# Performance work log

Measured on AMD Instinct MI355X. Metric: run time of the kernel, lower is better.

Reference implementation:

```python
import jax, jax.numpy as jnp
import numpy as np
from jax import lax

LSTM_UNITS = 64
BATCH = 2048
TIMESTEPS = 1024


def _lstm_cell(x, h, c, W_ih, W_hh, b_ih, b_hh):
    # PyTorch LSTMCell gate order: i, f, g, o
    gates = x @ W_ih.T + b_ih + h @ W_hh.T + b_hh
    i, f, g, o = jnp.split(gates, 4, axis=-1)
    c_new = jax.nn.sigmoid(f) * c + jax.nn.sigmoid(i) * jnp.tanh(g)
    h_new = jax.nn.sigmoid(o) * jnp.tanh(c_new)
    return h_new, c_new


def setup_inputs() -> dict:
    key = jax.random.key(0)
    ks = jax.random.split(key, 9)
    U = LSTM_UNITS
    s0 = 1.0 / np.sqrt(U)  # torch LSTMCell init scale (hidden=64)
    s1 = 1.0  # hidden=1 -> scale 1/sqrt(1)
    inp = {
        "input": jax.random.normal(ks[0], (BATCH, TIMESTEPS), dtype=jnp.float32),
        # c0: LSTMCell(1, 64)
        "W_ih0": jax.random.uniform(ks[1], (4 * U, 1), jnp.float32, -s0, s0),
        "W_hh0": jax.random.uniform(ks[2], (4 * U, U), jnp.float32, -s0, s0),
        "b_ih0": jax.random.uniform(ks[3], (4 * U,), jnp.float32, -s0, s0),
        "b_hh0": jax.random.uniform(ks[4], (4 * U,), jnp.float32, -s0, s0),
        # c1: LSTMCell(64, 1)
        "W_ih1": jax.random.uniform(ks[5], (4, U), jnp.float32, -s1, s1),
        "W_hh1": jax.random.uniform(ks[6], (4, 1), jnp.float32, -s1, s1),
        "b_ih1": jax.random.uniform(ks[7], (4,), jnp.float32, -s1, s1),
        "b_hh1": jax.random.uniform(ks[8], (4,), jnp.float32, -s1, s1),
    }
    return inp


def reference(input, W_ih0, W_hh0, b_ih0, b_hh0, W_ih1, W_hh1, b_ih1, b_hh1):
    B = input.shape[0]
    U = LSTM_UNITS
    dt = input.dtype
    h0 = jnp.zeros((B, U), dt)
    c0 = jnp.zeros((B, U), dt)
    h1 = jnp.zeros((B, 1), dt)
    c1 = jnp.zeros((B, 1), dt)

    def step(carry, x_t):
        h0, c0, h1, c1 = carry
        h0n, c0n = _lstm_cell(x_t, h0, c0, W_ih0, W_hh0, b_ih0, b_hh0)
        # NOTE: the original feeds the CELL state c0n (not h0n) into layer 2
        h1n, c1n = _lstm_cell(c0n, h1, c1, W_ih1, W_hh1, b_ih1, b_hh1)
        # output per step is the cell state of layer 2
        return (h0n, c0n, h1n, c1n), c1n

    xs = input.T[:, :, None]  # (T, B, 1)
    _, ys = lax.scan(step, (h0, c0, h1, c1), xs)  # ys: (T, B, 1)
    return ys[:, :, 0].T  # (B, T)
```

## Files before the change

kernel.cpp:

```cpp
#include <hip/hip_runtime.h>

#define T_STEPS 1024
#define BATCH 2048
#define BTILE 4
#define HS 36

typedef short short8 __attribute__((ext_vector_type(8)));
typedef float f32x4 __attribute__((ext_vector_type(4)));
typedef float f32x2 __attribute__((ext_vector_type(2)));

__device__ __forceinline__ float fast_rcp(float x) {
#if __has_builtin(__builtin_amdgcn_rcpf)
    return __builtin_amdgcn_rcpf(x);
#else
    return 1.0f / x;
#endif
}

__device__ __forceinline__ float fast_exp2(float x) {
#if __has_builtin(__builtin_amdgcn_exp2f)
    return __builtin_amdgcn_exp2f(x);
#else
    return exp2f(x);
#endif
}

__device__ __forceinline__ float sigf(float x) {
    return fast_rcp(1.0f + fast_exp2(-1.44269504f * x));
}

__device__ __forceinline__ f32x2 sigf2(f32x2 v) {
    f32x2 t = v * (-1.44269504f);
    f32x2 e = {fast_exp2(t[0]), fast_exp2(t[1])};
    e = e + 1.0f;
    return f32x2{fast_rcp(e[0]), fast_rcp(e[1])};
}

__device__ __forceinline__ float tanh_fast(float x) {
    float e = fast_exp2(2.88539008f * x);
    return 1.0f - 2.0f * fast_rcp(e + 1.0f);
}

__device__ __forceinline__ unsigned f2bf(float x) {
    unsigned u = __float_as_uint(x);
    unsigned r = u + 0x7FFFu + ((u >> 16) & 1u);
    return r >> 16;
}
__device__ __forceinline__ float bf2f(unsigned b) {
    return __uint_as_float(b << 16);
}

__device__ __forceinline__ unsigned cvt_pk_bf16(float a, float b) {
    unsigned r;
    asm("v_cvt_pk_bf16_f32 %0, %1, %2" : "=v"(r) : "v"(a), "v"(b));
    return r;
}

__device__ __forceinline__ float sel4A(f32x4 a) {
    int v = __float_as_int(a[0]);
    v = __builtin_amdgcn_update_dpp(v, __float_as_int(a[1]), 0x114, 0xf, 0x2, false);
    v = __builtin_amdgcn_update_dpp(v, __float_as_int(a[2]), 0x118, 0xf, 0x4, false);
    v = __builtin_amdgcn_update_dpp(v, __float_as_int(a[3]), 0x11C, 0xf, 0x8, false);
    return __int_as_float(v);
}
__device__ __forceinline__ float dpp_shl4f(float v) {
    return __int_as_float(__builtin_amdgcn_update_dpp(0, __float_as_int(v), 0x104, 0xf, 0xf, true));
}

__device__ __forceinline__ void step_barrier() {
    asm volatile("s_waitcnt lgkmcnt(0)" ::: "memory");
    __builtin_amdgcn_s_barrier();
    asm volatile("" ::: "memory");
}

__global__ __launch_bounds__(256, 2)
void lstm_v9_kernel(const float* __restrict__ input,
                    const float* __restrict__ W_ih0,
                    const float* __restrict__ W_hh0,
                    const float* __restrict__ b_ih0,
                    const float* __restrict__ b_hh0,
                    const float* __restrict__ W_ih1,
                    const float* __restrict__ W_hh1,
                    const float* __restrict__ b_ih1,
                    const float* __restrict__ b_hh1,
                    float* __restrict__ out)
{
    const int tid = threadIdx.x;
    const int w   = tid >> 6;
    const int l   = tid & 63;
    const int q16 = l >> 4;
    const int n16 = l & 15;
    const int nb  = l & 3;
    const int r   = (l >> 2) & 3;
    const int u   = 16 * w + 4 * q16 + r;
    const int bbase = blockIdx.x * BTILE;

    __shared__ __align__(16) unsigned Hbuf[2][3][16][HS];
    __shared__ float Xb[2][BTILE][65];
    __shared__ float Lst[8];

    for (int i = tid; i < 2 * 3 * 16 * HS; i += 256)
        reinterpret_cast<unsigned*>(Hbuf)[i] = 0u;
    if (tid < 8) Lst[tid] = 0.0f;

    short8 a1[4][2];
    #pragma unroll
    for (int g = 0; g < 4; ++g) {
        #pragma unroll
        for (int kt = 0; kt < 2; ++kt) {
            const float* p = W_hh0 + (size_t)(16 * (w + 4 * g) + n16) * 64 + kt * 32 + q16 * 8;
            short8 a;
            #pragma unroll
            for (int j = 0; j < 8; ++j) a[j] = (short)f2bf(p[j]);
            a1[g][kt] = a;
        }
    }
    short8 a2h[2], a2l[2];
    #pragma unroll
    for (int kt = 0; kt < 2; ++kt) {
        short8 ah = {0,0,0,0,0,0,0,0}, al = {0,0,0,0,0,0,0,0};
        if (n16 < 4) {
            const float* p = W_ih1 + (size_t)n16 * 64 + kt * 32 + q16 * 8;
            #pragma unroll
            for (int j = 0; j < 8; ++j) {
                unsigned hb = f2bf(p[j]);
                ah[j] = (short)hb;
                al[j] = (short)f2bf(p[j] - bf2f(hb));
            }
        }
        a2h[kt] = ah; a2l[kt] = al;
    }

    f32x2 w01, w23, b01, b23;
    {
        float wgv[4], bgv[4];
        #pragma unroll
        for (int g = 0; g < 4; ++g) {
            int row = g * 64 + u;
            wgv[g] = W_ih0[row];
            bgv[g] = b_ih0[row] + b_hh0[row];
        }
        w01 = f32x2{wgv[0], wgv[1]}; w23 = f32x2{wgv[2], wgv[3]};
        b01 = f32x2{bgv[0], bgv[1]}; b23 = f32x2{bgv[2], bgv[3]};
    }
    float whh1v[4], b1v[4];
    #pragma unroll
    for (int g = 0; g < 4; ++g) { whh1v[g] = W_hh1[g]; b1v[g] = b_ih1[g] + b_hh1[g]; }

    const float* inrow = input + (size_t)(bbase + w) * T_STEPS;
    Xb[0][w][l] = inrow[l];
    float xnext = 0.0f;
    float c0 = 0.0f;

    __syncthreads();

    if (blockIdx.x & 256) {
        __builtin_amdgcn_s_sleep(5);
    }

    int par = 0;
    #pragma unroll 2
    for (int t = 0; t < T_STEPS; ++t) {
        if ((t & 63) == 0 && t + 64 < T_STEPS) xnext = inrow[t + 64 + l];
        const int cp = (t >> 6) & 1;

        const unsigned* Hrow = &Hbuf[par][0][n16][0];
        short8 hb0 = *reinterpret_cast<const short8*>(Hrow + 4 * q16);
        short8 hb1 = *reinterpret_cast<const short8*>(Hrow + 16 + 4 * q16);

        f32x4 accv[4];
        #pragma unroll
        for (int g = 0; g < 4; ++g) {
            f32x4 z = {0.0f, 0.0f, 0.0f, 0.0f};
            z = __builtin_amdgcn_mfma_f32_16x16x32_bf16(a1[g][0], hb0, z, 0, 0, 0);
            z = __builtin_amdgcn_mfma_f32_16x16x32_bf16(a1[g][1], hb1, z, 0, 0, 0);
            accv[g] = z;
        }

        if (t > 0 && w == ((t - 1) & 3)) {
            const unsigned* Ch = &Hbuf[par][1][n16][0];
            const unsigned* Cl = &Hbuf[par][2][n16][0];
            short8 ch0 = *reinterpret_cast<const short8*>(Ch + 4 * q16);
            short8 ch1 = *reinterpret_cast<const short8*>(Ch + 16 + 4 * q16);
            short8 cl0 = *reinterpret_cast<const short8*>(Cl + 4 * q16);
            short8 cl1 = *reinterpret_cast<const short8*>(Cl + 16 + 4 * q16);
            float h1p = Lst[nb], c1p = Lst[4 + nb];
            f32x4 zA = {0.0f, 0.0f, 0.0f, 0.0f};
            f32x4 zB = {0.0f, 0.0f, 0.0f, 0.0f};
            zA = __builtin_amdgcn_mfma_f32_16x16x32_bf16(a2h[0], ch0, zA, 0, 0, 0);
            zB = __builtin_amdgcn_mfma_f32_16x16x32_bf16(a2l[1], ch1, zB, 0, 0, 0);
            zA = __builtin_amdgcn_mfma_f32_16x16x32_bf16(a2h[1], ch1, zA, 0, 0, 0);
            zB = __builtin_amdgcn_mfma_f32_16x16x32_bf16(a2h[0], cl0, zB, 0, 0, 0);
            zA = __builtin_amdgcn_mfma_f32_16x16x32_bf16(a2l[0], ch0, zA, 0, 0, 0);
            zB = __builtin_amdgcn_mfma_f32_16x16x32_bf16(a2h[1], cl1, zB, 0, 0, 0);
            f32x4 z = zA + zB;
            float g1i = z[0] + b1v[0] + h1p * whh1v[0];
            float g1f = z[1] + b1v[1] + h1p * whh1v[1];
            float g1g = z[2] + b1v[2] + h1p * whh1v[2];
            float g1o = z[3] + b1v[3] + h1p * whh1v[3];
            float c1n = sigf(g1f) * c1p + sigf(g1i) * tanh_fast(g1g);
            float h1n = sigf(g1o) * tanh_fast(c1n);
            if (l < 4) {
                out[(size_t)(bbase + l) * T_STEPS + (t - 1)] = c1n;
                Lst[l] = h1n;
                Lst[4 + l] = c1n;
            }
        }

        float g4[4];
        #pragma unroll
        for (int g = 0; g < 4; ++g) g4[g] = sel4A(accv[g]);

        float x = Xb[cp][nb][t & 63];
        f32x2 xx = {x, x};
        f32x2 gif = f32x2{g4[0], g4[1]} + (xx * w01 + b01);
        f32x2 ggo = f32x2{g4[2], g4[3]} + (xx * w23 + b23);

        f32x2 sif = sigf2(gif);
        float tg  = tanh_fast(ggo[0]);
        float c0n = sif[1] * c0 + sif[0] * tg;
        c0 = c0n;
        float h0n = sigf(ggo[1]) * tanh_fast(c0n);

        float ph = dpp_shl4f(h0n);
        float pc = dpp_shl4f(c0n);
        unsigned hword  = cvt_pk_bf16(h0n, ph);
        unsigned chword = cvt_pk_bf16(c0n, pc);
        float hi_own = bf2f(chword & 0xFFFFu);
        float lo_own = c0n - hi_own;
        float plo = dpp_shl4f(lo_own);
        unsigned clword = cvt_pk_bf16(lo_own, plo);
        if (!(l & 4)) {
            int widx = 8 * w + 2 * q16 + (r >> 1);
            Hbuf[par ^ 1][0][nb][widx] = hword;
            Hbuf[par ^ 1][1][nb][widx] = chword;
            Hbuf[par ^ 1][2][nb][widx] = clword;
        }
        if ((t & 63) == 63 && t + 1 < T_STEPS) Xb[cp ^ 1][w][l] = xnext;

        step_barrier();
        par ^= 1;
    }

    if (w == 3) {
        const unsigned* Ch = &Hbuf[par][1][n16][0];
        const unsigned* Cl = &Hbuf[par][2][n16][0];
        short8 ch0 = *reinterpret_cast<const short8*>(Ch + 4 * q16);
        short8 ch1 = *reinterpret_cast<const short8*>(Ch + 16 + 4 * q16);
        short8 cl0 = *reinterpret_cast<const short8*>(Cl + 4 * q16);
        short8 cl1 = *reinterpret_cast<const short8*>(Cl + 16 + 4 * q16);
        float h1p = Lst[nb], c1p = Lst[4 + nb];
        f32x4 zA = {0.0f, 0.0f, 0.0f, 0.0f};
        f32x4 zB = {0.0f, 0.0f, 0.0f, 0.0f};
        zA = __builtin_amdgcn_mfma_f32_16x16x32_bf16(a2h[0], ch0, zA, 0, 0, 0);
        zB = __builtin_amdgcn_mfma_f32_16x16x32_bf16(a2l[1], ch1, zB, 0, 0, 0);
        zA = __builtin_amdgcn_mfma_f32_16x16x32_bf16(a2h[1], ch1, zA, 0, 0, 0);
        zB = __builtin_amdgcn_mfma_f32_16x16x32_bf16(a2h[0], cl0, zB, 0, 0, 0);
        zA = __builtin_amdgcn_mfma_f32_16x16x32_bf16(a2l[0], ch0, zA, 0, 0, 0);
        zB = __builtin_amdgcn_mfma_f32_16x16x32_bf16(a2h[1], cl1, zB, 0, 0, 0);
        f32x4 z = zA + zB;
        float g1i = z[0] + b1v[0] + h1p * whh1v[0];
        float g1f = z[1] + b1v[1] + h1p * whh1v[1];
        float g1g = z[2] + b1v[2] + h1p * whh1v[2];
        float g1o = z[3] + b1v[3] + h1p * whh1v[3];
        float c1n = sigf(g1f) * c1p + sigf(g1i) * tanh_fast(g1g);
        if (l < 4)
            out[(size_t)(bbase + l) * T_STEPS + (T_STEPS - 1)] = c1n;
    }
}

extern "C" void kernel_launch(void* const* d_in, const int* in_sizes, int n_in,
                              void* d_out, int out_size, void* d_ws, size_t ws_size,
                              hipStream_t stream) {
    const float* input = (const float*)d_in[0];
    const float* W_ih0 = (const float*)d_in[1];
    const float* W_hh0 = (const float*)d_in[2];
    const float* b_ih0 = (const float*)d_in[3];
    const float* b_hh0 = (const float*)d_in[4];
    const float* W_ih1 = (const float*)d_in[5];
    const float* W_hh1 = (const float*)d_in[6];
    const float* b_ih1 = (const float*)d_in[7];
    const float* b_hh1 = (const float*)d_in[8];
    float* out = (float*)d_out;

    dim3 grid(BATCH / BTILE);
    dim3 block(256);
    lstm_v9_kernel<<<grid, block, 0, stream>>>(
        input, W_ih0, W_hh0, b_ih0, b_hh0, W_ih1, W_hh1, b_ih1, b_hh1, out);
}
```

Before: 536.7 us.

## Process two interleaved 4-row batch groups per block to hide recurrence latency

Each block now handles 8 batch rows as two independent 4-row streams (A and B) with separate LDS buffers. Their MFMAs and gate math are interleaved so each stream's dependency chain can hide the other's latency. The grid is halved to 256 blocks, launch bounds drop to one block per CU, and the staggered start sleep is removed. Layer-2 work for stream B runs on a different wave than stream A to spread it out. This trades the old two-blocks-per-CU occupancy for instruction-level parallelism inside one block, with higher register pressure.

```diff
diff --git a/kernel.cpp b/kernel.cpp
--- a/kernel.cpp
+++ b/kernel.cpp
@@ -2,7 +2,7 @@
 
 #define T_STEPS 1024
 #define BATCH 2048
-#define BTILE 4
+#define BTILE 8
 #define HS 36
 
 typedef short short8 __attribute__((ext_vector_type(8)));
@@ -73,17 +73,53 @@
     asm volatile("" ::: "memory");
 }
 
-__global__ __launch_bounds__(256, 2)
-void lstm_v9_kernel(const float* __restrict__ input,
-                    const float* __restrict__ W_ih0,
-                    const float* __restrict__ W_hh0,
-                    const float* __restrict__ b_ih0,
-                    const float* __restrict__ b_hh0,
-                    const float* __restrict__ W_ih1,
-                    const float* __restrict__ W_hh1,
-                    const float* __restrict__ b_ih1,
-                    const float* __restrict__ b_hh1,
-                    float* __restrict__ out)
+__device__ __forceinline__ void layer2(const unsigned (*Hb)[16][HS],
+                                       float* Lst,
+                                       const short8* a2h, const short8* a2l,
+                                       const float* whh1v, const float* b1v,
+                                       int n16, int q16, int nb, int l,
+                                       float* out, int bb, int tout)
+{
+    const unsigned* Ch = &Hb[1][n16][0];
+    const unsigned* Cl = &Hb[2][n16][0];
+    short8 ch0 = *reinterpret_cast<const short8*>(Ch + 4 * q16);
+    short8 ch1 = *reinterpret_cast<const short8*>(Ch + 16 + 4 * q16);
+    short8 cl0 = *reinterpret_cast<const short8*>(Cl + 4 * q16);
+    short8 cl1 = *reinterpret_cast<const short8*>(Cl + 16 + 4 * q16);
+    float h1p = Lst[nb], c1p = Lst[4 + nb];
+    f32x4 zA = {0.0f, 0.0f, 0.0f, 0.0f};
+    f32x4 zB = {0.0f, 0.0f, 0.0f, 0.0f};
+    zA = __builtin_amdgcn_mfma_f32_16x16x32_bf16(a2h[0], ch0, zA, 0, 0, 0);
+    zB = __builtin_amdgcn_mfma_f32_16x16x32_bf16(a2l[1], ch1, zB, 0, 0, 0);
+    zA = __builtin_amdgcn_mfma_f32_16x16x32_bf16(a2h[1], ch1, zA, 0, 0, 0);
+    zB = __builtin_amdgcn_mfma_f32_16x16x32_bf16(a2h[0], cl0, zB, 0, 0, 0);
+    zA = __builtin_amdgcn_mfma_f32_16x16x32_bf16(a2l[0], ch0, zA, 0, 0, 0);
+    zB = __builtin_amdgcn_mfma_f32_16x16x32_bf16(a2h[1], cl1, zB, 0, 0, 0);
+    f32x4 z = zA + zB;
+    float g1i = z[0] + b1v[0] + h1p * whh1v[0];
+    float g1f = z[1] + b1v[1] + h1p * whh1v[1];
+    float g1g = z[2] + b1v[2] + h1p * whh1v[2];
+    float g1o = z[3] + b1v[3] + h1p * whh1v[3];
+    float c1n = sigf(g1f) * c1p + sigf(g1i) * tanh_fast(g1g);
+    float h1n = sigf(g1o) * tanh_fast(c1n);
+    if (l < 4) {
+        out[(size_t)(bb + l) * T_STEPS + tout] = c1n;
+        Lst[l] = h1n;
+        Lst[4 + l] = c1n;
+    }
+}
+
+__global__ __launch_bounds__(256, 1)
+void lstm_v10_kernel(const float* __restrict__ input,
+                     const float* __restrict__ W_ih0,
+                     const float* __restrict__ W_hh0,
+                     const float* __restrict__ b_ih0,
+                     const float* __restrict__ b_hh0,
+                     const float* __restrict__ W_ih1,
+                     const float* __restrict__ W_hh1,
+                     const float* __restrict__ b_ih1,
+                     const float* __restrict__ b_hh1,
+                     float* __restrict__ out)
 {
     const int tid = threadIdx.x;
     const int w   = tid >> 6;
@@ -95,13 +131,17 @@
     const int u   = 16 * w + 4 * q16 + r;
     const int bbase = blockIdx.x * BTILE;
 
-    __shared__ __align__(16) unsigned Hbuf[2][3][16][HS];
-    __shared__ float Xb[2][BTILE][65];
-    __shared__ float Lst[8];
-
-    for (int i = tid; i < 2 * 3 * 16 * HS; i += 256)
-        reinterpret_cast<unsigned*>(Hbuf)[i] = 0u;
-    if (tid < 8) Lst[tid] = 0.0f;
+    __shared__ __align__(16) unsigned HbufA[2][3][16][HS];
+    __shared__ __align__(16) unsigned HbufB[2][3][16][HS];
+    __shared__ float XbA[2][4][65];
+    __shared__ float XbB[2][4][65];
+    __shared__ float LstA[8], LstB[8];
+
+    for (int i = tid; i < 2 * 3 * 16 * HS; i += 256) {
+        reinterpret_cast<unsigned*>(HbufA)[i] = 0u;
+        reinterpret_cast<unsigned*>(HbufB)[i] = 0u;
+    }
+    if (tid < 8) { LstA[tid] = 0.0f; LstB[tid] = 0.0f; }
 
     short8 a1[4][2];
     #pragma unroll
@@ -147,126 +187,117 @@
     #pragma unroll
     for (int g = 0; g < 4; ++g) { whh1v[g] = W_hh1[g]; b1v[g] = b_ih1[g] + b_hh1[g]; }
 
-    const float* inrow = input + (size_t)(bbase + w) * T_STEPS;
-    Xb[0][w][l] = inrow[l];
-    float xnext = 0.0f;
-    float c0 = 0.0f;
+    const float* inrowA = input + (size_t)(bbase + w) * T_STEPS;
+    const float* inrowB = input + (size_t)(bbase + 4 + w) * T_STEPS;
+    XbA[0][w][l] = inrowA[l];
+    XbB[0][w][l] = inrowB[l];
+    float xnextA = 0.0f, xnextB = 0.0f;
+    float c0A = 0.0f, c0B = 0.0f;
 
     __syncthreads();
-
-    if (blockIdx.x & 256) {
-        __builtin_amdgcn_s_sleep(5);
-    }
 
     int par = 0;
     #pragma unroll 2
     for (int t = 0; t < T_STEPS; ++t) {
-        if ((t & 63) == 0 && t + 64 < T_STEPS) xnext = inrow[t + 64 + l];
+        if ((t & 63) == 0 && t + 64 < T_STEPS) {
+            xnextA = inrowA[t + 64 + l];
+            xnextB = inrowB[t + 64 + l];
+        }
         const int cp = (t >> 6) & 1;
 
-        const unsigned* Hrow = &Hbuf[par][0][n16][0];
-        short8 hb0 = *reinterpret_cast<const short8*>(Hrow + 4 * q16);
-        short8 hb1 = *reinterpret_cast<const short8*>(Hrow + 16 + 4 * q16);
-
-        f32x4 accv[4];
+        const unsigned* HrA = &HbufA[par][0][n16][0];
+        const unsigned* HrB = &HbufB[par][0][n16][0];
+        short8 hb0A = *reinterpret_cast<const short8*>(HrA + 4 * q16);
+        short8 hb1A = *reinterpret_cast<const short8*>(HrA + 16 + 4 * q16);
+        short8 hb0B = *reinterpret_cast<const short8*>(HrB + 4 * q16);
+        short8 hb1B = *reinterpret_cast<const short8*>(HrB + 16 + 4 * q16);
+
+        f32x4 accA[4], accB[4];
         #pragma unroll
         for (int g = 0; g < 4; ++g) {
-            f32x4 z = {0.0f, 0.0f, 0.0f, 0.0f};
-            z = __builtin_amdgcn_mfma_f32_16x16x32_bf16(a1[g][0], hb0, z, 0, 0, 0);
-            z = __builtin_amdgcn_mfma_f32_16x16x32_bf16(a1[g][1], hb1, z, 0, 0, 0);
-            accv[g] = z;
-        }
-
-        if (t > 0 && w == ((t - 1) & 3)) {
-            const unsigned* Ch = &Hbuf[par][1][n16][0];
-            const unsigned* Cl = &Hbuf[par][2][n16][0];
-            short8 ch0 = *reinterpret_cast<const short8*>(Ch + 4 * q16);
-            short8 ch1 = *reinterpret_cast<const short8*>(Ch + 16 + 4 * q16);
-            short8 cl0 = *reinterpret_cast<const short8*>(Cl + 4 * q16);
-            short8 cl1 = *reinterpret_cast<const short8*>(Cl + 16 + 4 * q16);
-            float h1p = Lst[nb], c1p = Lst[4 + nb];
             f32x4 zA = {0.0f, 0.0f, 0.0f, 0.0f};
             f32x4 zB = {0.0f, 0.0f, 0.0f, 0.0f};
-            zA = __builtin_amdgcn_mfma_f32_16x16x32_bf16(a2h[0], ch0, zA, 0, 0, 0);
-            zB = __builtin_amdgcn_mfma_f32_16x16x32_bf16(a2l[1], ch1, zB, 0, 0, 0);
-            zA = __builtin_amdgcn_mfma_f32_16x16x32_bf16(a2h[1], ch1, zA, 0, 0, 0);
-            zB = __builtin_amdgcn_mfma_f32_16x16x32_bf16(a2h[0], cl0, zB, 0, 0, 0);
-            zA = __builtin_amdgcn_mfma_f32_16x16x32_bf16(a2l[0], ch0, zA, 0, 0, 0);
-            zB = __builtin_amdgcn_mfma_f32_16x16x32_bf16(a2h[1], cl1, zB, 0, 0, 0);
-            f32x4 z = zA + zB;
-            float g1i = z[0] + b1v[0] + h1p * whh1v[0];
-            float g1f = z[1] + b1v[1] + h1p * whh1v[1];
-            float g1g = z[2] + b1v[2] + h1p * whh1v[2];
-            float g1o = z[3] + b1v[3] + h1p * whh1v[3];
-            float c1n = sigf(g1f) * c1p + sigf(g1i) * tanh_fast(g1g);
-            float h1n = sigf(g1o) * tanh_fast(c1n);
-            if (l < 4) {
-                out[(size_t)(bbase + l) * T_STEPS + (t - 1)] = c1n;
-                Lst[l] = h1n;
-                Lst[4 + l] = c1n;
-            }
-        }
-
-        float g4[4];
+            zA = __builtin_amdgcn_mfma_f32_16x16x32_bf16(a1[g][0], hb0A, zA, 0, 0, 0);
+            zB = __builtin_amdgcn_mfma_f32_16x16x32_bf16(a1[g][0], hb0B, zB, 0, 0, 0);
+            zA = __builtin_amdgcn_mfma_f32_16x16x32_bf16(a1[g][1], hb1A, zA, 0, 0, 0);
+            zB = __builtin_amdgcn_mfma_f32_16x16x32_bf16(a1[g][1], hb1B, zB, 0, 0, 0);
+            accA[g] = zA; accB[g] = zB;
+        }
+
+        if (t > 0) {
+            const int lw = (t - 1) & 3;
+            if (w == lw)
+                layer2(HbufA[par], LstA, a2h, a2l, whh1v, b1v,
+                       n16, q16, nb, l, out, bbase, t - 1);
+            if (w == (lw ^ 2))
+                layer2(HbufB[par], LstB, a2h, a2l, whh1v, b1v,
+                       n16, q16, nb, l, out, bbase + 4, t - 1);
+        }
+
+        float g4A[4], g4B[4];
         #pragma unroll
-        for (int g = 0; g < 4; ++g) g4[g] = sel4A(accv[g]);
-
-        float x = Xb[cp][nb][t & 63];
-        f32x2 xx = {x, x};
-        f32x2 gif = f32x2{g4[0], g4[1]} + (xx * w01 + b01);
-        f32x2 ggo = f32x2{g4[2], g4[3]} + (xx * w23 + b23);
-
-        f32x2 sif = sigf2(gif);
-        float tg  = tanh_fast(ggo[0]);
-        float c0n = sif[1] * c0 + sif[0] * tg;
-        c0 = c0n;
-        float h0n = sigf(ggo[1]) * tanh_fast(c0n);
-
-        float ph = dpp_shl4f(h0n);
-        float pc = dpp_shl4f(c0n);
-        unsigned hword  = cvt_pk_bf16(h0n, ph);
-        unsigned chword = cvt_pk_bf16(c0n, pc);
-        float hi_own = bf2f(chword & 0xFFFFu);
-        float lo_own = c0n - hi_own;
-        float plo = dpp_shl4f(lo_own);
-        unsigned clword = cvt_pk_bf16(lo_own, plo);
+        for (int g = 0; g < 4; ++g) { g4A[g] = sel4A(accA[g]); g4B[g] = sel4A(accB[g]); }
+
+        float xA = XbA[cp][nb][t & 63];
+        float xB = XbB[cp][nb][t & 63];
+        f32x2 xxA = {xA, xA}, xxB = {xB, xB};
+        f32x2 gifA = f32x2{g4A[0], g4A[1]} + (xxA * w01 + b01);
+        f32x2 ggoA = f32x2{g4A[2], g4A[3]} + (xxA * w23 + b23);
+        f32x2 gifB = f32x2{g4B[0], g4B[1]} + (xxB * w01 + b01);
+        f32x2 ggoB = f32x2{g4B[2], g4B[3]} + (xxB * w23 + b23);
+
+        f32x2 sifA = sigf2(gifA);
+        f32x2 sifB = sigf2(gifB);
+        float tgA = tanh_fast(ggoA[0]);
+        float tgB = tanh_fast(ggoB[0]);
+        float c0nA = sifA[1] * c0A + sifA[0] * tgA;
+        float c0nB = sifB[1] * c0B + sifB[0] * tgB;
+        c0A = c0nA; c0B = c0nB;
+        float h0nA = sigf(ggoA[1]) * tanh_fast(c0nA);
+        float h0nB = sigf(ggoB[1]) * tanh_fast(c0nB);
+
+        float phA = dpp_shl4f(h0nA);
+        float pcA = dpp_shl4f(c0nA);
+        unsigned hwordA  = cvt_pk_bf16(h0nA, phA);
+        unsigned chwordA = cvt_pk_bf16(c0nA, pcA);
+        float hi_ownA = bf2f(chwordA & 0xFFFFu);
+        float lo_ownA = c0nA - hi_ownA;
+        float plolA = dpp_shl4f(lo_ownA);
+        unsigned clwordA = cvt_pk_bf16(lo_ownA, plolA);
+
+        float phB = dpp_shl4f(h0nB);
+        float pcB = dpp_shl4f(c0nB);
+        unsigned hwordB  = cvt_pk_bf16(h0nB, phB);
+        unsigned chwordB = cvt_pk_bf16(c0nB, pcB);
+        float hi_ownB = bf2f(chwordB & 0xFFFFu);
+        float lo_ownB = c0nB - hi_ownB;
+        float plolB = dpp_shl4f(lo_ownB);
+        unsigned clwordB = cvt_pk_bf16(lo_ownB, plolB);
+
         if (!(l & 4)) {
             int widx = 8 * w + 2 * q16 + (r >> 1);
-            Hbuf[par ^ 1][0][nb][widx] = hword;
-            Hbuf[par ^ 1][1][nb][widx] = chword;
-            Hbuf[par ^ 1][2][nb][widx] = clword;
-        }
-        if ((t & 63) == 63 && t + 1 < T_STEPS) Xb[cp ^ 1][w][l] = xnext;
+            HbufA[par ^ 1][0][nb][widx] = hwordA;
+            HbufA[par ^ 1][1][nb][widx] = chwordA;
+            HbufA[par ^ 1][2][nb][widx] = clwordA;
+            HbufB[par ^ 1][0][nb][widx] = hwordB;
+            HbufB[par ^ 1][1][nb][widx] = chwordB;
+            HbufB[par ^ 1][2][nb][widx] = clwordB;
+        }
+        if ((t & 63) == 63 && t + 1 < T_STEPS) {
+            XbA[cp ^ 1][w][l] = xnextA;
+            XbB[cp ^ 1][w][l] = xnextB;
+        }
 
         step_barrier();
         par ^= 1;
     }
 
-    if (w == 3) {
-        const unsigned* Ch = &Hbuf[par][1][n16][0];
-        const unsigned* Cl = &Hbuf[par][2][n16][0];
-        short8 ch0 = *reinterpret_cast<const short8*>(Ch + 4 * q16);
-        short8 ch1 = *reinterpret_cast<const short8*>(Ch + 16 + 4 * q16);
-        short8 cl0 = *reinterpret_cast<const short8*>(Cl + 4 * q16);
-        short8 cl1 = *reinterpret_cast<const short8*>(Cl + 16 + 4 * q16);
-        float h1p = Lst[nb], c1p = Lst[4 + nb];
-        f32x4 zA = {0.0f, 0.0f, 0.0f, 0.0f};
-        f32x4 zB = {0.0f, 0.0f, 0.0f, 0.0f};
-        zA = __builtin_amdgcn_mfma_f32_16x16x32_bf16(a2h[0], ch0, zA, 0, 0, 0);
-        zB = __builtin_amdgcn_mfma_f32_16x16x32_bf16(a2l[1], ch1, zB, 0, 0, 0);
-        zA = __builtin_amdgcn_mfma_f32_16x16x32_bf16(a2h[1], ch1, zA, 0, 0, 0);
-        zB = __builtin_amdgcn_mfma_f32_16x16x32_bf16(a2h[0], cl0, zB, 0, 0, 0);
-        zA = __builtin_amdgcn_mfma_f32_16x16x32_bf16(a2l[0], ch0, zA, 0, 0, 0);
-        zB = __builtin_amdgcn_mfma_f32_16x16x32_bf16(a2h[1], cl1, zB, 0, 0, 0);
-        f32x4 z = zA + zB;
-        float g1i = z[0] + b1v[0] + h1p * whh1v[0];
-        float g1f = z[1] + b1v[1] + h1p * whh1v[1];
-        float g1g = z[2] + b1v[2] + h1p * whh1v[2];
-        float g1o = z[3] + b1v[3] + h1p * whh1v[3];
-        float c1n = sigf(g1f) * c1p + sigf(g1i) * tanh_fast(g1g);
-        if (l < 4)
-            out[(size_t)(bbase + l) * T_STEPS + (T_STEPS - 1)] = c1n;
-    }
+    if (w == 3)
+        layer2(HbufA[par], LstA, a2h, a2l, whh1v, b1v,
+               n16, q16, nb, l, out, bbase, T_STEPS - 1);
+    if (w == 1)
+        layer2(HbufB[par], LstB, a2h, a2l, whh1v, b1v,
+               n16, q16, nb, l, out, bbase + 4, T_STEPS - 1);
 }
 
 extern "C" void kernel_launch(void* const* d_in, const int* in_sizes, int n_in,
@@ -285,6 +316,6 @@
 
     dim3 grid(BATCH / BTILE);
     dim3 block(256);
-    lstm_v9_kernel<<<grid, block, 0, stream>>>(
+    lstm_v10_kernel<<<grid, block, 0, stream>>>(
         input, W_ih0, W_hh0, b_ih0, b_hh0, W_ih1, W_hh1, b_ih1, b_hh1, out);
 }
```

Result: slower. 798.8 us (+48.9%).

## Defer layer-2 cell compute by one step to overlap with layer-1 MFMAs

Applied to the files above, without the earlier changes.

The layer-2 LSTM cell work is split into two phases. At step t-1 a wave only loads the cell-state fragments into registers. At step t it runs the layer-2 MFMAs and activations, placed before the layer-1 MFMAs. This takes the LDS read latency off the critical path of the step that loads the data, and gives the scheduler independent work to interleave with the main recurrence. In exchange it holds extra registers across the barrier and adds epilogue handling with an extra barrier.

```diff
diff --git a/kernel.cpp b/kernel.cpp
--- a/kernel.cpp
+++ b/kernel.cpp
@@ -73,17 +73,51 @@
     asm volatile("" ::: "memory");
 }
 
+__device__ __forceinline__ void layer2_compute(short8 ch0, short8 ch1,
+                                               short8 cl0, short8 cl1,
+                                               float* Lst,
+                                               const short8* a2h, const short8* a2l,
+                                               const float* whh1v, const float* b1v,
+                                               int nb, int l,
+                                               float* __restrict__ out, int bb, int tout,
+                                               bool writeLst)
+{
+    float h1p = Lst[nb], c1p = Lst[4 + nb];
+    f32x4 zA = {0.0f, 0.0f, 0.0f, 0.0f};
+    f32x4 zB = {0.0f, 0.0f, 0.0f, 0.0f};
+    zA = __builtin_amdgcn_mfma_f32_16x16x32_bf16(a2h[0], ch0, zA, 0, 0, 0);
+    zB = __builtin_amdgcn_mfma_f32_16x16x32_bf16(a2l[1], ch1, zB, 0, 0, 0);
+    zA = __builtin_amdgcn_mfma_f32_16x16x32_bf16(a2h[1], ch1, zA, 0, 0, 0);
+    zB = __builtin_amdgcn_mfma_f32_16x16x32_bf16(a2h[0], cl0, zB, 0, 0, 0);
+    zA = __builtin_amdgcn_mfma_f32_16x16x32_bf16(a2l[0], ch0, zA, 0, 0, 0);
+    zB = __builtin_amdgcn_mfma_f32_16x16x32_bf16(a2h[1], cl1, zB, 0, 0, 0);
+    f32x4 z = zA + zB;
+    float g1i = z[0] + b1v[0] + h1p * whh1v[0];
+    float g1f = z[1] + b1v[1] + h1p * whh1v[1];
+    float g1g = z[2] + b1v[2] + h1p * whh1v[2];
+    float g1o = z[3] + b1v[3] + h1p * whh1v[3];
+    float c1n = sigf(g1f) * c1p + sigf(g1i) * tanh_fast(g1g);
+    float h1n = sigf(g1o) * tanh_fast(c1n);
+    if (l < 4) {
+        out[(size_t)(bb + l) * T_STEPS + tout] = c1n;
+        if (writeLst) {
+            Lst[l] = h1n;
+            Lst[4 + l] = c1n;
+        }
+    }
+}
+
 __global__ __launch_bounds__(256, 2)
-void lstm_v9_kernel(const float* __restrict__ input,
-                    const float* __restrict__ W_ih0,
-                    const float* __restrict__ W_hh0,
-                    const float* __restrict__ b_ih0,
-                    const float* __restrict__ b_hh0,
-                    const float* __restrict__ W_ih1,
-                    const float* __restrict__ W_hh1,
-                    const float* __restrict__ b_ih1,
-                    const float* __restrict__ b_hh1,
-                    float* __restrict__ out)
+void lstm_v11_kernel(const float* __restrict__ input,
+                     const float* __restrict__ W_ih0,
+                     const float* __restrict__ W_hh0,
+                     const float* __restrict__ b_ih0,
+                     const float* __restrict__ b_hh0,
+                     const float* __restrict__ W_ih1,
+                     const float* __restrict__ W_hh1,
+                     const float* __restrict__ b_ih1,
+                     const float* __restrict__ b_hh1,
+                     float* __restrict__ out)
 {
     const int tid = threadIdx.x;
     const int w   = tid >> 6;
@@ -152,6 +186,9 @@
     float xnext = 0.0f;
     float c0 = 0.0f;
 
+    short8 r_ch0 = {0,0,0,0,0,0,0,0}, r_ch1 = {0,0,0,0,0,0,0,0};
+    short8 r_cl0 = {0,0,0,0,0,0,0,0}, r_cl1 = {0,0,0,0,0,0,0,0};
+
     __syncthreads();
 
     if (blockIdx.x & 256) {
@@ -167,6 +204,12 @@
         const unsigned* Hrow = &Hbuf[par][0][n16][0];
         short8 hb0 = *reinterpret_cast<const short8*>(Hrow + 4 * q16);
         short8 hb1 = *reinterpret_cast<const short8*>(Hrow + 16 + 4 * q16);
+
+        if (t >= 2 && w == ((t - 2) & 3)) {
+            layer2_compute(r_ch0, r_ch1, r_cl0, r_cl1, Lst,
+                           a2h, a2l, whh1v, b1v, nb, l,
+                           out, bbase, t - 2, true);
+        }
 
         f32x4 accv[4];
         #pragma unroll
@@ -177,34 +220,13 @@
             accv[g] = z;
         }
 
-        if (t > 0 && w == ((t - 1) & 3)) {
+        if (t >= 1 && w == ((t - 1) & 3)) {
             const unsigned* Ch = &Hbuf[par][1][n16][0];
             const unsigned* Cl = &Hbuf[par][2][n16][0];
-            short8 ch0 = *reinterpret_cast<const short8*>(Ch + 4 * q16);
-            short8 ch1 = *reinterpret_cast<const short8*>(Ch + 16 + 4 * q16);
-            short8 cl0 = *reinterpret_cast<const short8*>(Cl + 4 * q16);
-            short8 cl1 = *reinterpret_cast<const short8*>(Cl + 16 + 4 * q16);
-            float h1p = Lst[nb], c1p = Lst[4 + nb];
-            f32x4 zA = {0.0f, 0.0f, 0.0f, 0.0f};
-            f32x4 zB = {0.0f, 0.0f, 0.0f, 0.0f};
-            zA = __builtin_amdgcn_mfma_f32_16x16x32_bf16(a2h[0], ch0, zA, 0, 0, 0);
-            zB = __builtin_amdgcn_mfma_f32_16x16x32_bf16(a2l[1], ch1, zB, 0, 0, 0);
-            zA = __builtin_amdgcn_mfma_f32_16x16x32_bf16(a2h[1], ch1, zA, 0, 0, 0);
-            zB = __builtin_amdgcn_mfma_f32_16x16x32_bf16(a2h[0], cl0, zB, 0, 0, 0);
-            zA = __builtin_amdgcn_mfma_f32_16x16x32_bf16(a2l[0], ch0, zA, 0, 0, 0);
-            zB = __builtin_amdgcn_mfma_f32_16x16x32_bf16(a2h[1], cl1, zB, 0, 0, 0);
-            f32x4 z = zA + zB;
-            float g1i = z[0] + b1v[0] + h1p * whh1v[0];
-            float g1f = z[1] + b1v[1] + h1p * whh1v[1];
-            float g1g = z[2] + b1v[2] + h1p * whh1v[2];
-            float g1o = z[3] + b1v[3] + h1p * whh1v[3];
-            float c1n = sigf(g1f) * c1p + sigf(g1i) * tanh_fast(g1g);
-            float h1n = sigf(g1o) * tanh_fast(c1n);
-            if (l < 4) {
-                out[(size_t)(bbase + l) * T_STEPS + (t - 1)] = c1n;
-                Lst[l] = h1n;
-                Lst[4 + l] = c1n;
-            }
+            r_ch0 = *reinterpret_cast<const short8*>(Ch + 4 * q16);
+            r_ch1 = *reinterpret_cast<const short8*>(Ch + 16 + 4 * q16);
+            r_cl0 = *reinterpret_cast<const short8*>(Cl + 4 * q16);
+            r_cl1 = *reinterpret_cast<const short8*>(Cl + 16 + 4 * q16);
         }
 
         float g4[4];
@@ -242,6 +264,12 @@
         par ^= 1;
     }
 
+    if (w == 2) {
+        layer2_compute(r_ch0, r_ch1, r_cl0, r_cl1, Lst,
+                       a2h, a2l, whh1v, b1v, nb, l,
+                       out, bbase, T_STEPS - 2, true);
+    }
+    step_barrier();
     if (w == 3) {
         const unsigned* Ch = &Hbuf[par][1][n16][0];
         const unsigned* Cl = &Hbuf[par][2][n16][0];
@@ -249,23 +277,9 @@
         short8 ch1 = *reinterpret_cast<const short8*>(Ch + 16 + 4 * q16);
         short8 cl0 = *reinterpret_cast<const short8*>(Cl + 4 * q16);
         short8 cl1 = *reinterpret_cast<const short8*>(Cl + 16 + 4 * q16);
-        float h1p = Lst[nb], c1p = Lst[4 + nb];
-        f32x4 zA = {0.0f, 0.0f, 0.0f, 0.0f};
-        f32x4 zB = {0.0f, 0.0f, 0.0f, 0.0f};
-        zA = __builtin_amdgcn_mfma_f32_16x16x32_bf16(a2h[0], ch0, zA, 0, 0, 0);
-        zB = __builtin_amdgcn_mfma_f32_16x16x32_bf16(a2l[1], ch1, zB, 0, 0, 0);
-        zA = __builtin_amdgcn_mfma_f32_16x16x32_bf16(a2h[1], ch1, zA, 0, 0, 0);
-        zB = __builtin_amdgcn_mfma_f32_16x16x32_bf16(a2h[0], cl0, zB, 0, 0, 0);
-        zA = __builtin_amdgcn_mfma_f32_16x16x32_bf16(a2l[0], ch0, zA, 0, 0, 0);
-        zB = __builtin_amdgcn_mfma_f32_16x16x32_bf16(a2h[1], cl1, zB, 0, 0, 0);
-        f32x4 z = zA + zB;
-        float g1i = z[0] + b1v[0] + h1p * whh1v[0];
-        float g1f = z[1] + b1v[1] + h1p * whh1v[1];
-        float g1g = z[2] + b1v[2] + h1p * whh1v[2];
-        float g1o = z[3] + b1v[3] + h1p * whh1v[3];
-        float c1n = sigf(g1f) * c1p + sigf(g1i) * tanh_fast(g1g);
-        if (l < 4)
-            out[(size_t)(bbase + l) * T_STEPS + (T_STEPS - 1)] = c1n;
+        layer2_compute(ch0, ch1, cl0, cl1, Lst,
+                       a2h, a2l, whh1v, b1v, nb, l,
+                       out, bbase, T_STEPS - 1, false);
     }
 }
 
@@ -285,6 +299,6 @@
 
     dim3 grid(BATCH / BTILE);
     dim3 block(256);
-    lstm_v9_kernel<<<grid, block, 0, stream>>>(
+    lstm_v11_kernel<<<grid, block, 0, stream>>>(
         input, W_ih0, W_hh0, b_ih0, b_hh0, W_ih1, W_hh1, b_ih1, b_hh1, out);
 }
```

New measurement: 602.5 us. 1.12x slower.
